# Kernel optimization log

Hardware: AMD Instinct MI355X
Metric: run time of the kernel (lower is better)

The kernel has to match this reference:

```python
import jax, jax.numpy as jnp
import numpy as np

ENC, PRED, JOINT_H, VOCAB, BLANK, MAXSYM = 1024, 320, 512, 29, 28, 6


def _lstm_step(x, h, c, Wi, Wh, b):
    # torch LSTM gate order: i, f, g, o
    gates = x @ Wi.T + h @ Wh.T + b
    i, f, g, o = jnp.split(gates, 4, axis=-1)
    c2 = jax.nn.sigmoid(f) * c + jax.nn.sigmoid(i) * jnp.tanh(g)
    h2 = jax.nn.sigmoid(o) * jnp.tanh(c2)
    return h2, c2


def setup_inputs() -> dict:
    key = jax.random.key(0)
    ks = jax.random.split(key, 13)
    B, T = 32, 48
    s = 0.1
    return {
        "x": jax.random.normal(ks[0], (B, T, ENC), jnp.float32),
        "out_lens": jax.random.randint(ks[1], (B,), T // 2, T + 1),
        "emb": s * jax.random.normal(ks[2], (VOCAB - 1, PRED), jnp.float32),
        "Wi0": s * jax.random.normal(ks[3], (4 * PRED, PRED), jnp.float32),
        "Wh0": s * jax.random.normal(ks[4], (4 * PRED, PRED), jnp.float32),
        "b0": s * jax.random.normal(ks[5], (4 * PRED,), jnp.float32),
        "Wi1": s * jax.random.normal(ks[6], (4 * PRED, PRED), jnp.float32),
        "Wh1": s * jax.random.normal(ks[7], (4 * PRED, PRED), jnp.float32),
        "b1": s * jax.random.normal(ks[8], (4 * PRED,), jnp.float32),
        "Wj1": s * jax.random.normal(ks[9], (JOINT_H, ENC + PRED), jnp.float32),
        "bj1": s * jax.random.normal(ks[10], (JOINT_H,), jnp.float32),
        "Wj2": s * jax.random.normal(ks[11], (VOCAB, JOINT_H), jnp.float32),
        "bj2": s * jax.random.normal(ks[12], (VOCAB,), jnp.float32),
    }


def reference(x, out_lens, emb, Wi0, Wh0, b0, Wi1, Wh1, b1, Wj1, bj1, Wj2, bj2):
    B, T, _ = x.shape
    rows = jnp.arange(B)
    n_steps = T * MAXSYM  # upper bound on greedy-loop iterations

    def pred_step(label, h, c):
        # SOS (-1) -> zero embedding, matching model.prediction(None, ...)
        e = jnp.where((label >= 0)[:, None], emb[jnp.clip(label, 0)], 0.0)
        h0, c0 = _lstm_step(e, h[0], c[0], Wi0, Wh0, b0)
        h1, c1 = _lstm_step(h0, h[1], c[1], Wi1, Wh1, b1)
        return h1, jnp.stack([h0, h1]), jnp.stack([c0, c1])

    def joint(f, g):
        z = jnp.concatenate([f, g], axis=-1)  # [B, ENC+PRED]
        return jax.nn.relu(z @ Wj1.T + bj1) @ Wj2.T + bj2  # [B, VOCAB]

    def body(state, _):
        h, c, lt, lc, f, ti, sa = state
        last = lt[rows, lc]                      # last emitted symbol (or -1 = SOS)
        g, h_p, c_p = pred_step(last, h, c)
        logits = joint(f, g)
        k = jnp.argmax(logits, axis=-1).astype(jnp.int32)
        blankness = k == BLANK
        ti = ti + blankness.astype(jnp.int32)
        blank_vec = ti >= out_lens               # finished sequences
        sa = sa * (~blankness)                   # reset symbol count on blank
        not_blank = ~(blank_vec | blankness)
        # masked hidden-state scatter: hidden[:, idx, :] = hidden_prime[:, idx, :]
        h = jnp.where(not_blank[None, :, None], h_p, h)
        c = jnp.where(not_blank[None, :, None], c_p, c)
        lc = lc + not_blank.astype(jnp.int32)
        # index_put_ accumulate of (k - SOS) into label tensor initialized to SOS=-1
        lt = lt.at[rows, lc].add(jnp.where(not_blank, k + 1, 0))
        sa = sa + not_blank.astype(jnp.int32)
        need_add = sa >= MAXSYM                  # force time advance at max symbols
        ti = ti + need_add.astype(jnp.int32)
        sa = sa * (sa < MAXSYM)
        # data-dependent re-fetch of encoder frame (clamped like time_idxs.min(max_lens))
        f = x[rows, jnp.minimum(ti, T - 1)]
        return (h, c, lt, lc, f, ti, sa), None

    h0 = jnp.zeros((2, B, PRED), x.dtype)
    c0 = jnp.zeros((2, B, PRED), x.dtype)
    lt0 = jnp.full((B, n_steps), -1, jnp.int32)
    lc0 = jnp.zeros((B,), jnp.int32)
    ti0 = jnp.zeros((B,), jnp.int32)
    sa0 = jnp.zeros((B,), jnp.int32)
    f0 = x[:, 0, :]
    state, _ = jax.lax.scan(body, (h0, c0, lt0, lc0, f0, ti0, sa0), None, length=n_steps)
    _, _, lt, lc, _, _, _ = state
    # labels for item i are lt[i, 1:lc[i]+1]; return padded tensor + lengths
    return lt, lc
```

## Files before the change

### kernel.cpp

```cpp
#include <hip/hip_runtime.h>
#include <math.h>

#define B_ 32
#define T_ 48
#define ENC_ 1024
#define PRED_ 320
#define JH_ 512
#define NJ_ 1344
#define VOCAB_ 29
#define BLANK_ 28
#define MAXSYM_ 6
#define NSTEPS_ 288
#define BDEC 512
#define GRID_DEC 160
#define NG 8
#define GBAT 4
#define NBLK 20
#define JPB 16
#define NJB 16
#define VPB 32
#define HPAD 324

#define FPRE_OFF 0
#define WE_OFF   786432
#define H0C_OFF  822272
#define H1C_OFF  832512
#define PL_OFF   842752
#define INT_OFF  875520
#define NTAGS    10240

__device__ __forceinline__ float sigm(float v) { return 1.0f / (1.0f + expf(-v)); }

__device__ __forceinline__ int  ld_i(const int* p)   { return __hip_atomic_load((int*)p, __ATOMIC_RELAXED, __HIP_MEMORY_SCOPE_AGENT); }
__device__ __forceinline__ void st_i(int* p, int v)  { __hip_atomic_store(p, v, __ATOMIC_RELAXED, __HIP_MEMORY_SCOPE_AGENT); }
__device__ __forceinline__ void st_f(float* p, float v){ __hip_atomic_store(p, v, __ATOMIC_RELAXED, __HIP_MEMORY_SCOPE_AGENT); }

__device__ __forceinline__ void ldc4_1(const float* p0, float4& r0) {
    asm volatile("global_load_dwordx4 %0, %1, off sc0 sc1\n\t"
                 "s_waitcnt vmcnt(0)"
                 : "=v"(r0) : "v"(p0) : "memory");
}
__device__ __forceinline__ void ldc4_4(const float* p0, const float* p1,
                                       const float* p2, const float* p3,
                                       float4& r0, float4& r1, float4& r2, float4& r3) {
    asm volatile("global_load_dwordx4 %0, %4, off sc0 sc1\n\t"
                 "global_load_dwordx4 %1, %5, off sc0 sc1\n\t"
                 "global_load_dwordx4 %2, %6, off sc0 sc1\n\t"
                 "global_load_dwordx4 %3, %7, off sc0 sc1\n\t"
                 "s_waitcnt vmcnt(0)"
                 : "=&v"(r0), "=&v"(r1), "=&v"(r2), "=&v"(r3)
                 : "v"(p0), "v"(p1), "v"(p2), "v"(p3)
                 : "memory");
}

#define PIDX(g, ks, jl, gb) ((((g)*8 + (ks))*16 + (jl))*4 + (gb))

__global__ void k_init(float* __restrict__ ws, int* __restrict__ out) {
    int idx = blockIdx.x * blockDim.x + threadIdx.x;
    int stride = gridDim.x * blockDim.x;
    int* wi = (int*)ws;
    for (int i = idx; i < NTAGS; i += stride) wi[INT_OFF + i] = 0;
    for (int i = idx; i < B_*NSTEPS_; i += stride) out[i] = -1;
    if (idx < B_) out[B_*NSTEPS_ + idx] = 0;
}

__global__ __launch_bounds__(256) void k_we(const float* __restrict__ emb,
                                            const float* __restrict__ Wi0,
                                            float* __restrict__ ws) {
    __shared__ float es[PRED_];
    int l = blockIdx.x / 5;
    int rq = blockIdx.x % 5;
    int t = threadIdx.x;
    if (t < PRED_) es[t] = emb[l*PRED_ + t];
    if (t + 256 < PRED_) es[t + 256] = emb[l*PRED_ + t + 256];
    __syncthreads();
    int r = rq*256 + t;
    const float4* wr = (const float4*)(Wi0 + (size_t)r*PRED_);
    float acc = 0.0f;
    #pragma unroll 4
    for (int k4 = 0; k4 < PRED_/4; ++k4) {
        float4 w = wr[k4];
        acc += w.x*es[4*k4] + w.y*es[4*k4+1] + w.z*es[4*k4+2] + w.w*es[4*k4+3];
    }
    ws[WE_OFF + l*(4*PRED_) + r] = acc;
}

__global__ __launch_bounds__(256) void k_fpre(const float* __restrict__ x,
                                              const float* __restrict__ Wj1,
                                              const float* __restrict__ bj1,
                                              float* __restrict__ ws) {
    __shared__ float As[B_][129];
    __shared__ float Bs[64][129];
    int tt = blockIdx.x >> 3;
    int jb = blockIdx.x & 7;
    int tid = threadIdx.x;
    int b = tid >> 3, jq = tid & 7;
    float acc[8] = {0,0,0,0,0,0,0,0};
    for (int kc = 0; kc < ENC_; kc += 128) {
        for (int i = tid; i < B_*128; i += 256) {
            int bb = i >> 7, kk = i & 127;
            As[bb][kk] = x[((size_t)bb*T_ + tt)*ENC_ + kc + kk];
        }
        for (int i = tid; i < 64*128; i += 256) {
            int jj = i >> 7, kk = i & 127;
            Bs[jj][kk] = Wj1[((size_t)(jb*64 + jj))*NJ_ + kc + kk];
        }
        __syncthreads();
        for (int kk = 0; kk < 128; ++kk) {
            float a = As[b][kk];
            #pragma unroll
            for (int u = 0; u < 8; ++u) acc[u] += a * Bs[jq*8 + u][kk];
        }
        __syncthreads();
    }
    #pragma unroll
    for (int u = 0; u < 8; ++u) {
        int j = jb*64 + jq*8 + u;
        ws[FPRE_OFF + ((size_t)b*T_ + tt)*JH_ + j] = acc[u] + bj1[j];
    }
}

__global__ __launch_bounds__(BDEC) void k_decode(
    const int* __restrict__ out_lens,
    const float* __restrict__ Wh0, const float* __restrict__ b0,
    const float* __restrict__ Wi1, const float* __restrict__ Wh1,
    const float* __restrict__ b1,
    const float* __restrict__ Wj1,
    const float* __restrict__ Wj2, const float* __restrict__ bj2,
    float* __restrict__ ws, int* __restrict__ out)
{
    const int tid = threadIdx.x;
    const int grp = blockIdx.x & 7;
    const int lb  = blockIdx.x >> 3;
    const int j0  = lb * JPB;
    const int v0  = lb * VPB;
    const int bb0 = grp * GBAT;

    float* H0Cg = ws + H0C_OFF + grp*1280;
    float* H1Cg = ws + H1C_OFF + grp*1280;
    float* PLg  = ws + PL_OFF  + grp*4096;
    const float* WE = ws + WE_OFF;
    const float* FP = ws + FPRE_OFF;
    int* wi = (int*)ws;
    int* tagA = wi + INT_OFF +    0 + grp*320;
    int* tagB = wi + INT_OFF + 2560 + grp*320;
    int* tagC = wi + INT_OFF + 5120 + grp*320;
    int* tagD = wi + INT_OFF + 7680 + grp*320;

    __shared__ __align__(16) float wi1_s[64*HPAD];
    __shared__ __align__(16) float hs0[GBAT*HPAD];
    __shared__ __align__(16) float hs1[GBAT*HPAD];
    __shared__ float parts[2048];
    __shared__ float parts2[2048];
    __shared__ float P0a[256], P0b[256], P1s[256];
    __shared__ float c0cur[64], c0cand[64], c1cur[64], c1cand[64];
    __shared__ float we_s[28][64];
    __shared__ float b0_s[64], b1_s[64], bj2_s[32];
    __shared__ float wj2t[VPB*33];
    __shared__ float jg_c[VPB*GBAT];
    __shared__ float hid_s[GBAT*33];
    __shared__ float logits_s[GBAT*33];
    __shared__ int ti_l[GBAT], last_l[GBAT], sa_l[GBAT], lc_l[GBAT], olen_s[GBAT];
    __shared__ unsigned s_masks[2];

    for (int i = tid; i < 64*PRED_; i += BDEC) {
        int r = i / PRED_, c = i % PRED_;
        int g = r >> 4, jj = r & 15;
        wi1_s[r*HPAD + c] = Wi1[((size_t)(g*PRED_ + j0 + jj))*PRED_ + c];
    }
    if (lb < NJB) {
        for (int i = tid; i < VPB*32; i += BDEC) {
            int v = i >> 5, l = i & 31;
            wj2t[v*33 + l] = (l < VOCAB_) ? Wj2[(size_t)l*JH_ + v0 + v] : 0.f;
        }
    }
    for (int i = tid; i < 28*64; i += BDEC) {
        int ls = i >> 6, r = i & 63;
        int g = r >> 4, jj = r & 15;
        we_s[ls][r] = WE[(size_t)ls*(4*PRED_) + g*PRED_ + j0 + jj];
    }
    if (tid < 64) {
        int g = tid >> 4, jj = tid & 15;
        b0_s[tid] = b0[g*PRED_ + j0 + jj];
        b1_s[tid] = b1[g*PRED_ + j0 + jj];
        c0cur[tid]=0.f; c0cand[tid]=0.f; c1cur[tid]=0.f; c1cand[tid]=0.f;
    }
    if (tid < VOCAB_) bj2_s[tid] = bj2[tid];
    if (tid < GBAT) {
        olen_s[tid] = out_lens[bb0 + tid];
        ti_l[tid] = 0; last_l[tid] = -1; sa_l[tid] = 0; lc_l[tid] = 0;
    }
    for (int i = tid; i < GBAT*HPAD; i += BDEC) { hs0[i] = 0.f; hs1[i] = 0.f; }
    if (tid < 256) P0a[tid] = 0.f;
    __syncthreads();

    const int gb  = tid & 3;
    const int jl  = (tid >> 2) & 15;
    const int ks  = tid >> 6;
    unsigned nbm = 0xfu, actm = 0xfu;

    for (int s = 0; s < NSTEPS_; ++s) {
        const int par = s & 1;

        float f_reg = 0.f;
        if (lb < NJB && tid < 128) {
            int v_ = tid & 31, g2_ = tid >> 5;
            if ((actm >> g2_) & 1) {
                int tm = min(ti_l[g2_], T_ - 1);
                f_reg = FP[((size_t)(bb0+g2_)*T_ + tm)*JH_ + v0 + v_];
            }
        }

        if (nbm) {
            if (tid < 64) {
                int g2 = tid & 3, jj = tid >> 2;
                if ((nbm >> g2) & 1) {
                    int ls = last_l[g2];
                    float gt[4];
                    #pragma unroll
                    for (int g = 0; g < 4; ++g) {
                        int r = g*16 + jj;
                        float v = P0a[r*4 + g2] + b0_s[r];
                        if (ls >= 0) v += we_s[ls][r];
                        gt[g] = v;
                    }
                    float cn = sigm(gt[1])*c0cur[tid] + sigm(gt[0])*tanhf(gt[2]);
                    float hn = sigm(gt[3])*tanhf(cn);
                    c0cand[tid] = cn;
                    st_f(&H0Cg[g2*PRED_ + j0 + jj], hn);
                }
            }
            __syncthreads();
            if (tid == 0) st_i(&tagA[lb*16], s + 1);

            {
                const float* hr = &hs1[gb*HPAD];
                int k0 = ks * 40;
                float a0=0.f,a1=0.f,a2=0.f,a3=0.f;
                const float* w0 = Wh1 + ((size_t)(0*PRED_ + j0 + jl))*PRED_;
                const float* w1 = Wh1 + ((size_t)(1*PRED_ + j0 + jl))*PRED_;
                const float* w2 = Wh1 + ((size_t)(2*PRED_ + j0 + jl))*PRED_;
                const float* w3 = Wh1 + ((size_t)(3*PRED_ + j0 + jl))*PRED_;
                #pragma unroll 10
                for (int kk = k0; kk < k0 + 40; kk += 4) {
                    float4 h = *(const float4*)&hr[kk];
                    float4 q0 = *(const float4*)(w0 + kk);
                    float4 q1 = *(const float4*)(w1 + kk);
                    float4 q2 = *(const float4*)(w2 + kk);
                    float4 q3 = *(const float4*)(w3 + kk);
                    a0 += q0.x*h.x+q0.y*h.y+q0.z*h.z+q0.w*h.w;
                    a1 += q1.x*h.x+q1.y*h.y+q1.z*h.z+q1.w*h.w;
                    a2 += q2.x*h.x+q2.y*h.y+q2.z*h.z+q2.w*h.w;
                    a3 += q3.x*h.x+q3.y*h.y+q3.z*h.z+q3.w*h.w;
                }
                parts[PIDX(0,ks,jl,gb)] = a0;
                parts[PIDX(1,ks,jl,gb)] = a1;
                parts[PIDX(2,ks,jl,gb)] = a2;
                parts[PIDX(3,ks,jl,gb)] = a3;
            }
            __syncthreads();
            if (tid < 256) {
                int r = tid >> 2, g2 = tid & 3;
                int g = r >> 4, jj = r & 15;
                float v = 0.f;
                #pragma unroll
                for (int k = 0; k < 8; ++k) v += parts[PIDX(g,k,jj,g2)];
                P1s[r*4 + g2] = v;
            }
            if (tid < NBLK) { while (ld_i(&tagA[tid*16]) < s+1) __builtin_amdgcn_s_sleep(1); }
            __syncthreads();
            if (tid < 320) {
                int g2 = tid / 80, col = (tid - g2*80) * 4;
                if ((nbm >> g2) & 1) {
                    float4 r0;
                    ldc4_1(H0Cg + tid*4, r0);
                    *(float4*)&hs0[g2*HPAD + col] = r0;
                }
            }
            __syncthreads();

            {
                const float* hr = &hs0[gb*HPAD];
                int k0 = ks * 40;
                float a0=0.f,a1=0.f,a2=0.f,a3=0.f;
                #pragma unroll 10
                for (int kk = k0; kk < k0 + 40; kk += 4) {
                    float4 h = *(const float4*)&hr[kk];
                    float4 q0 = *(const float4*)&wi1_s[(0*16+jl)*HPAD + kk];
                    float4 q1 = *(const float4*)&wi1_s[(1*16+jl)*HPAD + kk];
                    float4 q2 = *(const float4*)&wi1_s[(2*16+jl)*HPAD + kk];
                    float4 q3 = *(const float4*)&wi1_s[(3*16+jl)*HPAD + kk];
                    a0 += q0.x*h.x+q0.y*h.y+q0.z*h.z+q0.w*h.w;
                    a1 += q1.x*h.x+q1.y*h.y+q1.z*h.z+q1.w*h.w;
                    a2 += q2.x*h.x+q2.y*h.y+q2.z*h.z+q2.w*h.w;
                    a3 += q3.x*h.x+q3.y*h.y+q3.z*h.z+q3.w*h.w;
                }
                parts[PIDX(0,ks,jl,gb)] = a0;
                parts[PIDX(1,ks,jl,gb)] = a1;
                parts[PIDX(2,ks,jl,gb)] = a2;
                parts[PIDX(3,ks,jl,gb)] = a3;
            }
            __syncthreads();
            if (tid < 64) {
                int g2 = tid & 3, jj = tid >> 2;
                if ((nbm >> g2) & 1) {
                    float gt[4];
                    #pragma unroll
                    for (int g = 0; g < 4; ++g) {
                        int r = g*16 + jj;
                        float v = P1s[r*4 + g2] + b1_s[r];
                        #pragma unroll
                        for (int k = 0; k < 8; ++k) v += parts[PIDX(g,k,jj,g2)];
                        gt[g] = v;
                    }
                    float cn = sigm(gt[1])*c1cur[tid] + sigm(gt[0])*tanhf(gt[2]);
                    float hn = sigm(gt[3])*tanhf(cn);
                    c1cand[tid] = cn;
                    st_f(&H1Cg[g2*PRED_ + j0 + jj], hn);
                }
            }
            __syncthreads();
            if (tid == 0) st_i(&tagB[lb*16], s + 1);

            {
                const float* hr = &hs0[gb*HPAD];
                int k0 = ks * 40;
                float a0=0.f,a1=0.f,a2=0.f,a3=0.f;
                const float* w0 = Wh0 + ((size_t)(0*PRED_ + j0 + jl))*PRED_;
                const float* w1 = Wh0 + ((size_t)(1*PRED_ + j0 + jl))*PRED_;
                const float* w2 = Wh0 + ((size_t)(2*PRED_ + j0 + jl))*PRED_;
                const float* w3 = Wh0 + ((size_t)(3*PRED_ + j0 + jl))*PRED_;
                #pragma unroll 10
                for (int kk = k0; kk < k0 + 40; kk += 4) {
                    float4 h = *(const float4*)&hr[kk];
                    float4 q0 = *(const float4*)(w0 + kk);
                    float4 q1 = *(const float4*)(w1 + kk);
                    float4 q2 = *(const float4*)(w2 + kk);
                    float4 q3 = *(const float4*)(w3 + kk);
                    a0 += q0.x*h.x+q0.y*h.y+q0.z*h.z+q0.w*h.w;
                    a1 += q1.x*h.x+q1.y*h.y+q1.z*h.z+q1.w*h.w;
                    a2 += q2.x*h.x+q2.y*h.y+q2.z*h.z+q2.w*h.w;
                    a3 += q3.x*h.x+q3.y*h.y+q3.z*h.z+q3.w*h.w;
                }
                parts2[PIDX(0,ks,jl,gb)] = a0;
                parts2[PIDX(1,ks,jl,gb)] = a1;
                parts2[PIDX(2,ks,jl,gb)] = a2;
                parts2[PIDX(3,ks,jl,gb)] = a3;
            }
            if (tid < NBLK) { while (ld_i(&tagB[tid*16]) < s+1) __builtin_amdgcn_s_sleep(1); }
            __syncthreads();
            if (tid < 320) {
                int g2 = tid / 80, col = (tid - g2*80) * 4;
                if ((nbm >> g2) & 1) {
                    float4 r0;
                    ldc4_1(H1Cg + tid*4, r0);
                    *(float4*)&hs1[g2*HPAD + col] = r0;
                }
            }
            __syncthreads();
        } else {
            if (lb < NJB) {
                if (tid < NBLK) { while (ld_i(&tagD[tid*16]) < s-1) __builtin_amdgcn_s_sleep(1); }
                __syncthreads();
            }
        }

        if (lb < NJB) {
            if (nbm) {
                int v = tid & 31, g2 = (tid >> 5) & 3, ks2 = tid >> 7;
                if ((nbm >> g2) & 1) {
                    const float* hr = &hs1[g2*HPAD];
                    const float* wt = Wj1 + ((size_t)(v0 + v))*NJ_ + ENC_ + ks2*80;
                    const float* hk = hr + ks2*80;
                    float p = 0.f;
                    #pragma unroll 20
                    for (int kk = 0; kk < 80; kk += 4) {
                        float4 w4 = *(const float4*)(wt + kk);
                        float4 h  = *(const float4*)(hk + kk);
                        p += w4.x*h.x + w4.y*h.y + w4.z*h.z + w4.w*h.w;
                    }
                    parts[(v*4 + g2)*4 + ks2] = p;
                }
            }
            __syncthreads();
            if (tid < 128) {
                int v = tid & 31, g2 = tid >> 5;
                if (nbm && ((nbm >> g2) & 1)) {
                    jg_c[v*4 + g2] = parts[(v*4+g2)*4+0] + parts[(v*4+g2)*4+1]
                                   + parts[(v*4+g2)*4+2] + parts[(v*4+g2)*4+3];
                }
                if ((actm >> g2) & 1) {
                    hid_s[g2*33 + v] = fmaxf(f_reg + jg_c[v*4 + g2], 0.f);
                }
            }
            __syncthreads();
            if (tid < 128) {
                int g2 = tid >> 5, l = tid & 31;
                const float* hb = &hid_s[g2*33];
                float acc = 0.f;
                #pragma unroll 8
                for (int v = 0; v < VPB; ++v) acc += wj2t[v*33 + l] * hb[v];
                st_f(&PLg[par*2048 + lb*128 + tid], acc);
            }
            __syncthreads();
            if (tid == 0) st_i(&tagC[lb*16], s + 1);
        }

        if (nbm && tid < 256) {
            int r = tid >> 2, g2 = tid & 3;
            int g = r >> 4, jj = r & 15;
            float v = 0.f;
            #pragma unroll
            for (int k = 0; k < 8; ++k) v += parts2[PIDX(g,k,jj,g2)];
            P0b[r*4 + g2] = v;
        }

        if (tid < NJB) { while (ld_i(&tagC[tid*16]) < s+1) __builtin_amdgcn_s_sleep(1); }
        __syncthreads();
        if (tid < 128) {
            int jq = tid >> 5, slot = tid & 31;
            const float* pb = PLg + par*2048 + (jq*4)*128 + slot*4;
            float4 r0, r1, r2, r3;
            ldc4_4(pb, pb + 128, pb + 256, pb + 384, r0, r1, r2, r3);
            float4 sm;
            sm.x = ((r0.x + r1.x) + r2.x) + r3.x;
            sm.y = ((r0.y + r1.y) + r2.y) + r3.y;
            sm.z = ((r0.z + r1.z) + r2.z) + r3.z;
            sm.w = ((r0.w + r1.w) + r2.w) + r3.w;
            *(float4*)&parts[jq*128 + slot*4] = sm;
        }
        __syncthreads();
        if (tid < 32) {
            #pragma unroll
            for (int e = 0; e < 4; ++e) {
                int f = tid*4 + e;
                float v = ((parts[0*128+f] + parts[1*128+f])
                         + parts[2*128+f]) + parts[3*128+f];
                int g2 = f >> 5, l = f & 31;
                logits_s[g2*33 + l] = (l < VOCAB_) ? (v + bj2_s[l]) : -1e30f;
            }
        }
        __syncthreads();

        if (tid < 64) {
            bool nbb = false, actb = false;
            if (tid < GBAT && ((actm >> tid) & 1)) {
                const int g2 = tid;
                float best = -1e30f; int bi = 0;
                for (int l = 0; l < VOCAB_; ++l) {
                    float v = logits_s[g2*33 + l];
                    if (v > best) { best = v; bi = l; }
                }
                const int blankness = (bi == BLANK_) ? 1 : 0;
                int tiv = ti_l[g2] + blankness;
                if (tiv >= olen_s[g2]) {
                    ti_l[g2] = tiv;
                } else {
                    int notb = 1 - blankness;
                    int sav = blankness ? 0 : sa_l[g2];
                    int nl = last_l[g2];
                    int lcn = lc_l[g2];
                    if (notb) {
                        lcn += 1;
                        if (lb == g2) {
                            int bglob = bb0 + g2;
                            if (lcn < NSTEPS_) st_i(&out[bglob*NSTEPS_ + lcn], bi);
                            st_i(&out[B_*NSTEPS_ + bglob], lcn);
                        }
                        nl = bi;
                        sav += 1;
                    }
                    if (sav >= MAXSYM_) { tiv += 1; sav = 0; }
                    ti_l[g2] = tiv; sa_l[g2] = sav; last_l[g2] = nl; lc_l[g2] = lcn;
                    nbb = (notb != 0); actb = true;
                }
            }
            unsigned long long bn = __ballot(nbb);
            unsigned long long ba = __ballot(actb);
            if (tid == 0) { s_masks[0] = (unsigned)bn; s_masks[1] = (unsigned)ba; }
        }
        __syncthreads();
        const unsigned nbm_new = s_masks[0];
        actm = s_masks[1];
        if (tid < 64) {
            if ((nbm_new >> (tid & 3)) & 1) { c0cur[tid] = c0cand[tid]; c1cur[tid] = c1cand[tid]; }
        }
        if (tid < 256) {
            if ((nbm_new >> (tid & 3)) & 1) P0a[tid] = P0b[tid];
        }
        __syncthreads();
        nbm = nbm_new;
        if (tid == 0) st_i(&tagD[lb*16], s + 1);
        if (!actm) break;
    }
}

extern "C" void kernel_launch(void* const* d_in, const int* in_sizes, int n_in,
                              void* d_out, int out_size, void* d_ws, size_t ws_size,
                              hipStream_t stream) {
    const float* x    = (const float*)d_in[0];
    const int*   olen = (const int*)d_in[1];
    const float* emb  = (const float*)d_in[2];
    const float* Wi0  = (const float*)d_in[3];
    const float* Wh0  = (const float*)d_in[4];
    const float* b0   = (const float*)d_in[5];
    const float* Wi1  = (const float*)d_in[6];
    const float* Wh1  = (const float*)d_in[7];
    const float* b1   = (const float*)d_in[8];
    const float* Wj1  = (const float*)d_in[9];
    const float* bj1  = (const float*)d_in[10];
    const float* Wj2  = (const float*)d_in[11];
    const float* bj2  = (const float*)d_in[12];
    float* ws = (float*)d_ws;
    int* out = (int*)d_out;

    hipLaunchKernelGGL(k_init, dim3(256), dim3(256), 0, stream, ws, out);
    hipLaunchKernelGGL(k_we,   dim3(28*5), dim3(256), 0, stream, emb, Wi0, ws);
    hipLaunchKernelGGL(k_fpre, dim3(T_*8), dim3(256), 0, stream, x, Wj1, bj1, ws);
    hipLaunchKernelGGL(k_decode, dim3(GRID_DEC), dim3(BDEC), 0, stream,
                       olen, Wh0, b0, Wi1, Wh1, b1, Wj1, Wj2, bj2, ws, out);
}
```

Baseline: 4.643 ms.

## Replace flag-based inter-block barriers with stamped value pairs polled by consumers

Each value exchanged between blocks (LSTM hidden states and partial logits) is now written as a (value, step stamp) pair in one 8-byte store. Consumers poll those pairs directly instead of waiting on per-block tag counters after a __syncthreads and then reloading the data. This removes a block barrier and a separate tag round-trip at each of the three exchange points per step, and blocks keep their own slice locally in shared memory. In exchange the scratch buffers double in size, many more threads spin on global memory, and correctness relies on stamps being written in the same store as their data.

```diff
diff --git a/kernel.cpp b/kernel.cpp
--- a/kernel.cpp
+++ b/kernel.cpp
@@ -23,30 +23,38 @@
 
 #define FPRE_OFF 0
 #define WE_OFF   786432
-#define H0C_OFF  822272
-#define H1C_OFF  832512
-#define PL_OFF   842752
-#define INT_OFF  875520
-#define NTAGS    10240
+#define H0C2_OFF 822272
+#define H1C2_OFF 842752
+#define PL2_OFF  863232
+#define INT_OFF  928768
+#define NTAGS    2560
+#define STAMPF   106496
 
 __device__ __forceinline__ float sigm(float v) { return 1.0f / (1.0f + expf(-v)); }
 
 __device__ __forceinline__ int  ld_i(const int* p)   { return __hip_atomic_load((int*)p, __ATOMIC_RELAXED, __HIP_MEMORY_SCOPE_AGENT); }
 __device__ __forceinline__ void st_i(int* p, int v)  { __hip_atomic_store(p, v, __ATOMIC_RELAXED, __HIP_MEMORY_SCOPE_AGENT); }
-__device__ __forceinline__ void st_f(float* p, float v){ __hip_atomic_store(p, v, __ATOMIC_RELAXED, __HIP_MEMORY_SCOPE_AGENT); }
-
-__device__ __forceinline__ void ldc4_1(const float* p0, float4& r0) {
-    asm volatile("global_load_dwordx4 %0, %1, off sc0 sc1\n\t"
+
+__device__ __forceinline__ void st_pair(float* p, float v, int stamp) {
+    float2 x; x.x = v; x.y = __int_as_float(stamp);
+    asm volatile("global_store_dwordx2 %0, %1, off sc0 sc1" :: "v"(p), "v"(x) : "memory");
+}
+__device__ __forceinline__ void ldc4_2(const float* p0, const float* p1,
+                                       float4& r0, float4& r1) {
+    asm volatile("global_load_dwordx4 %0, %2, off sc0 sc1\n\t"
+                 "global_load_dwordx4 %1, %3, off sc0 sc1\n\t"
                  "s_waitcnt vmcnt(0)"
-                 : "=v"(r0) : "v"(p0) : "memory");
-}
-__device__ __forceinline__ void ldc4_4(const float* p0, const float* p1,
-                                       const float* p2, const float* p3,
-                                       float4& r0, float4& r1, float4& r2, float4& r3) {
-    asm volatile("global_load_dwordx4 %0, %4, off sc0 sc1\n\t"
-                 "global_load_dwordx4 %1, %5, off sc0 sc1\n\t"
-                 "global_load_dwordx4 %2, %6, off sc0 sc1\n\t"
-                 "global_load_dwordx4 %3, %7, off sc0 sc1\n\t"
+                 : "=&v"(r0), "=&v"(r1)
+                 : "v"(p0), "v"(p1)
+                 : "memory");
+}
+__device__ __forceinline__ void ld2x4(const float* p0, const float* p1,
+                                      const float* p2, const float* p3,
+                                      float2& r0, float2& r1, float2& r2, float2& r3) {
+    asm volatile("global_load_dwordx2 %0, %4, off sc0 sc1\n\t"
+                 "global_load_dwordx2 %1, %5, off sc0 sc1\n\t"
+                 "global_load_dwordx2 %2, %6, off sc0 sc1\n\t"
+                 "global_load_dwordx2 %3, %7, off sc0 sc1\n\t"
                  "s_waitcnt vmcnt(0)"
                  : "=&v"(r0), "=&v"(r1), "=&v"(r2), "=&v"(r3)
                  : "v"(p0), "v"(p1), "v"(p2), "v"(p3)
@@ -58,6 +66,7 @@
 __global__ void k_init(float* __restrict__ ws, int* __restrict__ out) {
     int idx = blockIdx.x * blockDim.x + threadIdx.x;
     int stride = gridDim.x * blockDim.x;
+    for (int i = idx; i < STAMPF; i += stride) ws[H0C2_OFF + i] = 0.0f;
     int* wi = (int*)ws;
     for (int i = idx; i < NTAGS; i += stride) wi[INT_OFF + i] = 0;
     for (int i = idx; i < B_*NSTEPS_; i += stride) out[i] = -1;
@@ -136,16 +145,13 @@
     const int v0  = lb * VPB;
     const int bb0 = grp * GBAT;
 
-    float* H0Cg = ws + H0C_OFF + grp*1280;
-    float* H1Cg = ws + H1C_OFF + grp*1280;
-    float* PLg  = ws + PL_OFF  + grp*4096;
+    float* H0C2g = ws + H0C2_OFF + grp*2560;
+    float* H1C2g = ws + H1C2_OFF + grp*2560;
+    float* PL2g  = ws + PL2_OFF  + grp*8192;
     const float* WE = ws + WE_OFF;
     const float* FP = ws + FPRE_OFF;
     int* wi = (int*)ws;
-    int* tagA = wi + INT_OFF +    0 + grp*320;
-    int* tagB = wi + INT_OFF + 2560 + grp*320;
-    int* tagC = wi + INT_OFF + 5120 + grp*320;
-    int* tagD = wi + INT_OFF + 7680 + grp*320;
+    int* tagD = wi + INT_OFF + grp*320;
 
     __shared__ __align__(16) float wi1_s[64*HPAD];
     __shared__ __align__(16) float hs0[GBAT*HPAD];
@@ -201,6 +207,7 @@
 
     for (int s = 0; s < NSTEPS_; ++s) {
         const int par = s & 1;
+        const int st = s + 1;
 
         float f_reg = 0.f;
         if (lb < NJB && tid < 128) {
@@ -227,12 +234,10 @@
                     float cn = sigm(gt[1])*c0cur[tid] + sigm(gt[0])*tanhf(gt[2]);
                     float hn = sigm(gt[3])*tanhf(cn);
                     c0cand[tid] = cn;
-                    st_f(&H0Cg[g2*PRED_ + j0 + jj], hn);
-                }
-            }
-            __syncthreads();
-            if (tid == 0) st_i(&tagA[lb*16], s + 1);
-
+                    hs0[g2*HPAD + j0 + jj] = hn;
+                    st_pair(&H0C2g[(lb*64 + tid)*2], hn, st);
+                }
+            }
             {
                 const float* hr = &hs1[gb*HPAD];
                 int k0 = ks * 40;
@@ -267,14 +272,26 @@
                 for (int k = 0; k < 8; ++k) v += parts[PIDX(g,k,jj,g2)];
                 P1s[r*4 + g2] = v;
             }
-            if (tid < NBLK) { while (ld_i(&tagA[tid*16]) < s+1) __builtin_amdgcn_s_sleep(1); }
-            __syncthreads();
-            if (tid < 320) {
-                int g2 = tid / 80, col = (tid - g2*80) * 4;
-                if ((nbm >> g2) & 1) {
-                    float4 r0;
-                    ldc4_1(H0Cg + tid*4, r0);
-                    *(float4*)&hs0[g2*HPAD + col] = r0;
+            {
+                int b = tid >> 4, jj = tid & 15;
+                if (tid < 320 && b != lb) {
+                    const bool n0=(nbm>>0)&1, n1=(nbm>>1)&1, n2=(nbm>>2)&1, n3=(nbm>>3)&1;
+                    const float* a0 = H0C2g + tid*8;
+                    const float* a1 = a0 + 4;
+                    float4 r0, r1;
+                    for (;;) {
+                        ldc4_2(a0, a1, r0, r1);
+                        bool ok = (!n0 || __float_as_int(r0.y)==st)
+                               && (!n1 || __float_as_int(r0.w)==st)
+                               && (!n2 || __float_as_int(r1.y)==st)
+                               && (!n3 || __float_as_int(r1.w)==st);
+                        if (ok) break;
+                        __builtin_amdgcn_s_sleep(1);
+                    }
+                    if (n0) hs0[0*HPAD + b*16 + jj] = r0.x;
+                    if (n1) hs0[1*HPAD + b*16 + jj] = r0.z;
+                    if (n2) hs0[2*HPAD + b*16 + jj] = r1.x;
+                    if (n3) hs0[3*HPAD + b*16 + jj] = r1.z;
                 }
             }
             __syncthreads();
@@ -316,12 +333,10 @@
                     float cn = sigm(gt[1])*c1cur[tid] + sigm(gt[0])*tanhf(gt[2]);
                     float hn = sigm(gt[3])*tanhf(cn);
                     c1cand[tid] = cn;
-                    st_f(&H1Cg[g2*PRED_ + j0 + jj], hn);
-                }
-            }
-            __syncthreads();
-            if (tid == 0) st_i(&tagB[lb*16], s + 1);
-
+                    hs1[g2*HPAD + j0 + jj] = hn;
+                    st_pair(&H1C2g[(lb*64 + tid)*2], hn, st);
+                }
+            }
             {
                 const float* hr = &hs0[gb*HPAD];
                 int k0 = ks * 40;
@@ -347,14 +362,26 @@
                 parts2[PIDX(2,ks,jl,gb)] = a2;
                 parts2[PIDX(3,ks,jl,gb)] = a3;
             }
-            if (tid < NBLK) { while (ld_i(&tagB[tid*16]) < s+1) __builtin_amdgcn_s_sleep(1); }
-            __syncthreads();
-            if (tid < 320) {
-                int g2 = tid / 80, col = (tid - g2*80) * 4;
-                if ((nbm >> g2) & 1) {
-                    float4 r0;
-                    ldc4_1(H1Cg + tid*4, r0);
-                    *(float4*)&hs1[g2*HPAD + col] = r0;
+            {
+                int b = tid >> 4, jj = tid & 15;
+                if (tid < 320 && b != lb) {
+                    const bool n0=(nbm>>0)&1, n1=(nbm>>1)&1, n2=(nbm>>2)&1, n3=(nbm>>3)&1;
+                    const float* a0 = H1C2g + tid*8;
+                    const float* a1 = a0 + 4;
+                    float4 r0, r1;
+                    for (;;) {
+                        ldc4_2(a0, a1, r0, r1);
+                        bool ok = (!n0 || __float_as_int(r0.y)==st)
+                               && (!n1 || __float_as_int(r0.w)==st)
+                               && (!n2 || __float_as_int(r1.y)==st)
+                               && (!n3 || __float_as_int(r1.w)==st);
+                        if (ok) break;
+                        __builtin_amdgcn_s_sleep(1);
+                    }
+                    if (n0) hs1[0*HPAD + b*16 + jj] = r0.x;
+                    if (n1) hs1[1*HPAD + b*16 + jj] = r0.z;
+                    if (n2) hs1[2*HPAD + b*16 + jj] = r1.x;
+                    if (n3) hs1[3*HPAD + b*16 + jj] = r1.z;
                 }
             }
             __syncthreads();
@@ -400,10 +427,8 @@
                 float acc = 0.f;
                 #pragma unroll 8
                 for (int v = 0; v < VPB; ++v) acc += wj2t[v*33 + l] * hb[v];
-                st_f(&PLg[par*2048 + lb*128 + tid], acc);
-            }
-            __syncthreads();
-            if (tid == 0) st_i(&tagC[lb*16], s + 1);
+                st_pair(&PL2g[par*4096 + (lb*128 + tid)*2], acc, st);
+            }
         }
 
         if (nbm && tid < 256) {
@@ -415,30 +440,23 @@
             P0b[r*4 + g2] = v;
         }
 
-        if (tid < NJB) { while (ld_i(&tagC[tid*16]) < s+1) __builtin_amdgcn_s_sleep(1); }
+        {
+            int lb4 = tid >> 7, slot = tid & 127;
+            const float* base = PL2g + par*4096 + (lb4*4*128 + slot)*2;
+            float2 q0, q1, q2, q3;
+            for (;;) {
+                ld2x4(base, base + 256, base + 512, base + 768, q0, q1, q2, q3);
+                if (__float_as_int(q0.y)==st && __float_as_int(q1.y)==st &&
+                    __float_as_int(q2.y)==st && __float_as_int(q3.y)==st) break;
+                __builtin_amdgcn_s_sleep(1);
+            }
+            parts[tid] = ((q0.x + q1.x) + q2.x) + q3.x;
+        }
         __syncthreads();
         if (tid < 128) {
-            int jq = tid >> 5, slot = tid & 31;
-            const float* pb = PLg + par*2048 + (jq*4)*128 + slot*4;
-            float4 r0, r1, r2, r3;
-            ldc4_4(pb, pb + 128, pb + 256, pb + 384, r0, r1, r2, r3);
-            float4 sm;
-            sm.x = ((r0.x + r1.x) + r2.x) + r3.x;
-            sm.y = ((r0.y + r1.y) + r2.y) + r3.y;
-            sm.z = ((r0.z + r1.z) + r2.z) + r3.z;
-            sm.w = ((r0.w + r1.w) + r2.w) + r3.w;
-            *(float4*)&parts[jq*128 + slot*4] = sm;
-        }
-        __syncthreads();
-        if (tid < 32) {
-            #pragma unroll
-            for (int e = 0; e < 4; ++e) {
-                int f = tid*4 + e;
-                float v = ((parts[0*128+f] + parts[1*128+f])
-                         + parts[2*128+f]) + parts[3*128+f];
-                int g2 = f >> 5, l = f & 31;
-                logits_s[g2*33 + l] = (l < VOCAB_) ? (v + bj2_s[l]) : -1e30f;
-            }
+            float v = ((parts[tid] + parts[128+tid]) + parts[256+tid]) + parts[384+tid];
+            int g2 = tid >> 5, l = tid & 31;
+            logits_s[g2*33 + l] = (l < VOCAB_) ? (v + bj2_s[l]) : -1e30f;
         }
         __syncthreads();
 
```

Result: faster. 4.422 ms (-4.8%).
